# Kernel optimization log

Hardware: AMD Instinct MI355X
Metric: run time of the kernel (lower is better)

## Reference

```python
import jax, jax.numpy as jnp
import numpy as np
from jax import lax

D_MODEL = 512
D_STATE = 16
D_CONV = 4
EXPAND = 2
D_INNER = EXPAND * D_MODEL          # 1024
DT_RANK = (D_MODEL + 15) // 16      # 32 (ceil(d_model/16))
BATCH = 8
SEQLEN = 2048


def _mamba_params(key):
    ks = jax.random.split(key, 6)
    s = 0.02
    return {
        'in_w':   jax.random.normal(ks[0], (2 * D_INNER, D_MODEL)) * s,
        'conv_w': jax.random.normal(ks[1], (D_INNER, D_CONV)) * s,
        'conv_b': jnp.zeros((D_INNER,)),
        'xp_w':   jax.random.normal(ks[2], (DT_RANK + 2 * D_STATE, D_INNER)) * s,
        'dt_w':   jax.random.normal(ks[3], (D_INNER, DT_RANK)) * s,
        'dt_b':   jax.random.uniform(ks[4], (D_INNER,), minval=-4.0, maxval=-2.0),
        'A_log':  jnp.log(jnp.tile(jnp.arange(1, D_STATE + 1, dtype=jnp.float32), (D_INNER, 1))),
        'Dp':     jnp.ones((D_INNER,)),
        'out_w':  jax.random.normal(ks[5], (D_MODEL, D_INNER)) * s,
    }


def setup_inputs() -> dict:
    key = jax.random.key(0)
    kx, kf, kb, kl1, kl2 = jax.random.split(key, 5)
    pf = _mamba_params(kf)
    pb = _mamba_params(kb)
    inp = {'x': jax.random.normal(kx, (BATCH, SEQLEN, D_MODEL), dtype=jnp.float32)}
    for name, v in pf.items():
        inp['f_' + name] = v
    for name, v in pb.items():
        inp['b_' + name] = v
    inp['lin_w'] = jax.random.normal(kl1, (D_MODEL, 2 * D_MODEL)) * 0.02
    inp['lin_b'] = jnp.zeros((D_MODEL,))
    return inp


def _mamba(x, in_w, conv_w, conv_b, xp_w, dt_w, dt_b, A_log, Dp, out_w):
    # x: (B, L, D_MODEL)
    Bsz = x.shape[0]
    xz = x @ in_w.T                                  # (B, L, 2*D_INNER)
    xi, z = jnp.split(xz, 2, axis=-1)
    # causal depthwise conv over time
    xc = jnp.transpose(xi, (0, 2, 1))                # (B, D_INNER, L)
    xc = lax.conv_general_dilated(
        xc, conv_w[:, None, :], (1,), [(D_CONV - 1, 0)],
        feature_group_count=D_INNER)
    xi = jax.nn.silu(jnp.transpose(xc + conv_b[None, :, None], (0, 2, 1)))
    # input-dependent SSM params
    dbl = xi @ xp_w.T                                # (B, L, DT_RANK + 2*N)
    dt = jax.nn.softplus(dbl[..., :DT_RANK] @ dt_w.T + dt_b)    # (B, L, D_INNER)
    Bm = dbl[..., DT_RANK:DT_RANK + D_STATE]                    # (B, L, N)
    Cm = dbl[..., DT_RANK + D_STATE:]                           # (B, L, N)
    A = -jnp.exp(A_log)                                         # (D_INNER, N)

    def step(h, inp):
        dt_t, B_t, C_t, x_t = inp                    # (B,Di), (B,N), (B,N), (B,Di)
        h = jnp.exp(dt_t[..., None] * A) * h + (dt_t * x_t)[..., None] * B_t[:, None, :]
        y = jnp.einsum('bdn,bn->bd', h, C_t)
        return h, y

    xs = (jnp.swapaxes(dt, 0, 1), jnp.swapaxes(Bm, 0, 1),
          jnp.swapaxes(Cm, 0, 1), jnp.swapaxes(xi, 0, 1))
    h0 = jnp.zeros((Bsz, D_INNER, D_STATE), dtype=x.dtype)
    _, ys = lax.scan(step, h0, xs)                   # ys: (L, B, D_INNER)
    y = jnp.swapaxes(ys, 0, 1) + xi * Dp
    y = y * jax.nn.silu(z)
    return y @ out_w.T                               # (B, L, D_MODEL)


def reference(x,
              f_in_w, f_conv_w, f_conv_b, f_xp_w, f_dt_w, f_dt_b, f_A_log, f_Dp, f_out_w,
              b_in_w, b_conv_w, b_conv_b, b_xp_w, b_dt_w, b_dt_b, b_A_log, b_Dp, b_out_w,
              lin_w, lin_b):
    y_fwd = _mamba(x, f_in_w, f_conv_w, f_conv_b, f_xp_w, f_dt_w, f_dt_b, f_A_log, f_Dp, f_out_w)
    y_bwd = _mamba(x[:, ::-1, :], b_in_w, b_conv_w, b_conv_b, b_xp_w, b_dt_w, b_dt_b,
                   b_A_log, b_Dp, b_out_w)[:, ::-1, :]
    y = jnp.concatenate([y_fwd, y_bwd], axis=-1)     # (B, L, 2*D_MODEL)
    return y @ lin_w.T + lin_b
```

## Files before the change

### kernel.cpp

```cpp
#include <hip/hip_runtime.h>
#include <cmath>

#define LSEQ 2048
#define NBATCH 8

typedef __attribute__((ext_vector_type(8))) short short8;
typedef __attribute__((ext_vector_type(4))) float f32x4;

__device__ __forceinline__ float silu_f(float x) {
    return x * __builtin_amdgcn_rcpf(1.0f + __expf(-x));
}
__device__ __forceinline__ float softplus_f(float x) {
    return fmaxf(x, 0.0f) + __logf(1.0f + __expf(-fabsf(x)));
}
__device__ __forceinline__ unsigned short f2bf(float f) {
    unsigned int u = __float_as_uint(f);
    u += 0x7FFFu + ((u >> 16) & 1u);
    return (unsigned short)(u >> 16);
}
__device__ __forceinline__ float bf2f(unsigned short h) {
    return __uint_as_float(((unsigned int)h) << 16);
}
__device__ __forceinline__ void gload_lds16(const void* g, void* l) {
    __builtin_amdgcn_global_load_lds((const __attribute__((address_space(1))) void*)g,
                                     (__attribute__((address_space(3))) void*)l, 16, 0, 0);
}

#if defined(__has_builtin)
#if __has_builtin(__builtin_amdgcn_exp2f)
#define EXP2F(x) __builtin_amdgcn_exp2f(x)
#endif
#endif
#ifndef EXP2F
#define EXP2F(x) __expf((x) * 0.69314718055994531f)
#endif

struct GemmPair {
    const unsigned short* A[2];
    const unsigned short* A2[2];
    const unsigned short* W[2];
    const float* bias[2];
    void* C[2];
    unsigned short* aux[2];
};

template<int WGM, int WGN, int OMODE, int DK, int XTRA>
__global__ __launch_bounds__(WGM* WGN * 64) void gemm_mfma(GemmPair gp, int lda, int ldw,
                                                           int ldc, int K)
{
    constexpr int NW = WGM * WGN;
    constexpr int TM = WGM * 64, TN = WGN * 64;
    __shared__ unsigned short As[TM * 32];
    __shared__ unsigned short Bs[TN * 32];
    const int dir = blockIdx.z;
    const unsigned short* A  = gp.A[dir];
    const unsigned short* A2 = gp.A2[dir];
    const unsigned short* W  = gp.W[dir];
    const float* bias        = gp.bias[dir];
    void* Cout               = gp.C[dir];
    unsigned short* aux      = gp.aux[dir];

    const int tid = threadIdx.x;
    const int wave = tid >> 6, lane = tid & 63;
    const int wm = wave / WGN, wn = wave % WGN;
    const int m0 = blockIdx.x * TM, n0 = blockIdx.y * TN;
    const int l15 = lane & 15, l4 = lane >> 4;
    const int srow = lane >> 2, schunk = (lane & 3) * 8;

    f32x4 acc[4][4] = {};

    for (int k0 = 0; k0 < K; k0 += 32) {
        __syncthreads();
        for (int s = wave; s < TM / 16; s += NW) {
            const int gr = m0 + s * 16 + srow;
            const unsigned short* g;
            if (DK != 0 && k0 >= DK)
                g = A2 + (size_t)(gr ^ (LSEQ - 1)) * lda + (k0 - DK) + schunk;
            else
                g = A + (size_t)gr * lda + k0 + schunk;
            gload_lds16(g, (char*)As + (size_t)s * 1024);
        }
        for (int s = wave; s < TN / 16; s += NW) {
            const int gr = n0 + s * 16 + srow;
            const unsigned short* g = W + (size_t)gr * ldw + k0 + schunk;
            gload_lds16(g, (char*)Bs + (size_t)s * 1024);
        }
        __syncthreads();
        short8 af[4], bfr[4];
#pragma unroll
        for (int mi = 0; mi < 4; ++mi)
            af[mi] = *(const short8*)&As[(wm * 64 + mi * 16 + l15) * 32 + l4 * 8];
#pragma unroll
        for (int ni = 0; ni < 4; ++ni)
            bfr[ni] = *(const short8*)&Bs[(wn * 64 + ni * 16 + l15) * 32 + l4 * 8];
#pragma unroll
        for (int mi = 0; mi < 4; ++mi)
#pragma unroll
            for (int ni = 0; ni < 4; ++ni)
                acc[mi][ni] = __builtin_amdgcn_mfma_f32_16x16x32_bf16(af[mi], bfr[ni], acc[mi][ni], 0, 0, 0);
    }

#pragma unroll
    for (int mi = 0; mi < 4; ++mi)
#pragma unroll
        for (int ni = 0; ni < 4; ++ni)
#pragma unroll
            for (int r = 0; r < 4; ++r) {
                const int row = m0 + wm * 64 + mi * 16 + l4 * 4 + r;
                const int col = n0 + wn * 64 + ni * 16 + l15;
                float v = acc[mi][ni][r];
                if (bias) v += bias[col];
                if (OMODE & 1) ((unsigned short*)Cout)[(size_t)row * ldc + col] = f2bf(v);
                else           ((float*)Cout)[(size_t)row * ldc + col] = v;
                if (XTRA) { if (col < 32) aux[(size_t)row * 32 + col] = f2bf(v); }
            }
}

__global__ __launch_bounds__(256) void combine_k(
    const float* __restrict__ lin_w, const float* __restrict__ owf,
    const float* __restrict__ owb, unsigned short* __restrict__ Wcomb)
{
    const int dir = blockIdx.z;
    const float* ow = dir ? owb : owf;
    const int lane = threadIdx.x & 63;
    const int wave = threadIdx.x >> 6;
    const int n = blockIdx.y * 4 + wave;
    const int d = blockIdx.x * 256 + lane * 4;
    float4 acc = {0.f, 0.f, 0.f, 0.f};
    const float* lrow = lin_w + (size_t)n * 1024 + dir * 512;
    for (int j = 0; j < 512; ++j) {
        const float s = lrow[j];
        const float4 v = *(const float4*)&ow[(size_t)j * 1024 + d];
        acc.x = fmaf(s, v.x, acc.x); acc.y = fmaf(s, v.y, acc.y);
        acc.z = fmaf(s, v.z, acc.z); acc.w = fmaf(s, v.w, acc.w);
    }
    ushort4 o;
    o.x = f2bf(acc.x); o.y = f2bf(acc.y); o.z = f2bf(acc.z); o.w = f2bf(acc.w);
    *(ushort4*)&Wcomb[(size_t)n * 2048 + dir * 1024 + d] = o;
}

struct CvtArgs { const float* s[6]; unsigned short* d[6]; int n[6]; };
__global__ __launch_bounds__(256) void cvt_k(CvtArgs a)
{
    const int sid = blockIdx.y;
    const float* s = a.s[sid];
    unsigned short* d = a.d[sid];
    const int n4 = a.n[sid] >> 2;
    for (int i = blockIdx.x * 256 + threadIdx.x; i < n4; i += gridDim.x * 256) {
        const float4 v = ((const float4*)s)[i];
        ushort4 o; o.x = f2bf(v.x); o.y = f2bf(v.y); o.z = f2bf(v.z); o.w = f2bf(v.w);
        ((ushort4*)d)[i] = o;
    }
}
__global__ __launch_bounds__(256) void cvtx_k(const float* __restrict__ s,
                                              unsigned short* __restrict__ d, int n4)
{
    for (int i = blockIdx.x * 256 + threadIdx.x; i < n4; i += gridDim.x * 256) {
        const float4 v = ((const float4*)s)[i];
        ushort4 o; o.x = f2bf(v.x); o.y = f2bf(v.y); o.z = f2bf(v.z); o.w = f2bf(v.w);
        ((ushort4*)d)[i] = o;
    }
}

__global__ __launch_bounds__(256) void conv_silu_k(
    const unsigned short* __restrict__ xz_f, const float* __restrict__ cw_f,
    const float* __restrict__ cb_f, unsigned short* __restrict__ xi_f,
    const unsigned short* __restrict__ xz_b, const float* __restrict__ cw_b,
    const float* __restrict__ cb_b, unsigned short* __restrict__ xi_b)
{
    const int dir = blockIdx.y;
    const unsigned short* xz = dir ? xz_b : xz_f;
    const float* cw = dir ? cw_b : cw_f;
    const float* cb = dir ? cb_b : cb_f;
    unsigned short* xi = dir ? xi_b : xi_f;

    const int bt = blockIdx.x;
    const int b = bt >> 11;
    const int t = bt & (LSEQ - 1);
    const int d = threadIdx.x << 2;

    float w[4][4];
#pragma unroll
    for (int i = 0; i < 4; ++i) {
        const float4 wr = *(const float4*)&cw[(d + i) * 4];
        w[i][0] = wr.x; w[i][1] = wr.y; w[i][2] = wr.z; w[i][3] = wr.w;
    }
    float4 acc = *(const float4*)&cb[d];
#pragma unroll
    for (int k = 0; k < 4; ++k) {
        const int row = dir ? (LSEQ - 1 - t) + 3 - k : t - 3 + k;
        if ((unsigned)row < (unsigned)LSEQ) {
            const ushort4 v = *(const ushort4*)&xz[(size_t)(b * LSEQ + row) * 2048 + d];
            acc.x += w[0][k] * bf2f(v.x); acc.y += w[1][k] * bf2f(v.y);
            acc.z += w[2][k] * bf2f(v.z); acc.w += w[3][k] * bf2f(v.w);
        }
    }
    ushort4 st;
    st.x = f2bf(silu_f(acc.x)); st.y = f2bf(silu_f(acc.y));
    st.z = f2bf(silu_f(acc.z)); st.w = f2bf(silu_f(acc.w));
    *(ushort4*)&xi[(size_t)(b * LSEQ + t) * 1024 + d] = st;
}

__device__ __forceinline__ float row_sum8(float x) {
    x += __int_as_float(__builtin_amdgcn_update_dpp(0, __float_as_int(x), 0xB1, 0xF, 0xF, true));
    x += __int_as_float(__builtin_amdgcn_update_dpp(0, __float_as_int(x), 0x4E, 0xF, 0xF, true));
    x += __int_as_float(__builtin_amdgcn_update_dpp(0, __float_as_int(x), 0x141, 0xF, 0xF, true));
    return x;
}

struct ScanPair {
    const unsigned short* dblh[2];
    const unsigned short* dtw[2];
    const float* dtb[2];
    unsigned short* xiy[2];
    const float* dbl[2];
    const unsigned short* xz[2];
    const float* Al[2];
    const float* Dp[2];
};

__global__ __launch_bounds__(256, 2) void scan_k(ScanPair sp)
{
    __shared__ float sxi[2][64][36];
    __shared__ float sdt[32][68], sdtx[32][68];
    __shared__ float sB2[8][140], sC2[8][140];
    __shared__ float sy[32][68];

    const int dir = blockIdx.z;
    const unsigned short* dblh = sp.dblh[dir];
    const unsigned short* dtw  = sp.dtw[dir];
    const float* dtb           = sp.dtb[dir];
    unsigned short* xiy        = sp.xiy[dir];
    const float* dbl           = sp.dbl[dir];
    const unsigned short* zz   = sp.xz[dir];
    const float* Al            = sp.Al[dir];
    const float* Dpp           = sp.Dp[dir];

    const int b = blockIdx.y, d0 = blockIdx.x << 5;
    const int tid = threadIdx.x;
    const int wave = tid >> 6, lane = tid & 63;
    const int l15 = lane & 15, l4 = lane >> 4;
    const int di = tid >> 3, np = tid & 7;
    const int lr = tid >> 2, lc = tid & 3;
    const bool lead = (np == 0);

    const float A0L = -expf(Al[(d0 + di) * 16 + np]) * 1.4426950408889634f;
    const float A1L = -expf(Al[(d0 + di) * 16 + np + 8]) * 1.4426950408889634f;

    const short8 dtwf0 = *(const short8*)&dtw[(size_t)(d0 + l15) * 32 + l4 * 8];
    const short8 dtwf1 = *(const short8*)&dtw[(size_t)(d0 + 16 + l15) * 32 + l4 * 8];
    const float dtb0 = dtb[d0 + l15], dtb1 = dtb[d0 + 16 + l15];

    float dpv[8];
#pragma unroll
    for (int i = 0; i < 8; ++i) dpv[i] = Dpp[d0 + lc * 8 + i];

    ushort4 pxi0, pxi1;
    float4 pB, pC;
    short8 pA;
    auto issue_loads = [&](int c) {
        const size_t r = (size_t)b * LSEQ + c * 64 + lr;
        pxi0 = *(const ushort4*)&xiy[r * 1024 + d0 + lc * 8];
        pxi1 = *(const ushort4*)&xiy[r * 1024 + d0 + lc * 8 + 4];
        pB   = *(const float4*)&dbl[r * 64 + 32 + lc * 4];
        pC   = *(const float4*)&dbl[r * 64 + 48 + lc * 4];
        pA   = *(const short8*)&dblh[(size_t)(b * LSEQ + c * 64 + wave * 16 + l15) * 32 + l4 * 8];
    };
    issue_loads(0);

    float h0 = 0.0f, h1 = 0.0f;
    for (int c = 0; c < LSEQ / 64; ++c) {
        const int t0 = c * 64;
        const int buf = c & 1;
        {
            float4 xa, xb;
            xa.x = bf2f(pxi0.x); xa.y = bf2f(pxi0.y); xa.z = bf2f(pxi0.z); xa.w = bf2f(pxi0.w);
            xb.x = bf2f(pxi1.x); xb.y = bf2f(pxi1.y); xb.z = bf2f(pxi1.z); xb.w = bf2f(pxi1.w);
            *(float4*)&sxi[buf][lr][lc * 8]     = xa;
            *(float4*)&sxi[buf][lr][lc * 8 + 4] = xb;
        }
        {
            const float bv[4] = {pB.x, pB.y, pB.z, pB.w};
            const float cv[4] = {pC.x, pC.y, pC.z, pC.w};
#pragma unroll
            for (int i = 0; i < 4; ++i) {
                const int n = lc * 4 + i;
                sB2[n & 7][lr * 2 + (n >> 3)] = bv[i];
                sC2[n & 7][lr * 2 + (n >> 3)] = cv[i];
            }
        }
        __syncthreads();
        {
            f32x4 z4 = {0.f, 0.f, 0.f, 0.f};
            f32x4 dacc0 = __builtin_amdgcn_mfma_f32_16x16x32_bf16(pA, dtwf0, z4, 0, 0, 0);
            f32x4 dacc1 = __builtin_amdgcn_mfma_f32_16x16x32_bf16(pA, dtwf1, z4, 0, 0, 0);
            const int tq = wave * 16 + l4 * 4;
            float4 xi0, xi1;
            xi0.x = sxi[buf][tq + 0][l15];      xi0.y = sxi[buf][tq + 1][l15];
            xi0.z = sxi[buf][tq + 2][l15];      xi0.w = sxi[buf][tq + 3][l15];
            xi1.x = sxi[buf][tq + 0][16 + l15]; xi1.y = sxi[buf][tq + 1][16 + l15];
            xi1.z = sxi[buf][tq + 2][16 + l15]; xi1.w = sxi[buf][tq + 3][16 + l15];
            float4 dv0, dv1, dx0, dx1;
            dv0.x = softplus_f(dacc0[0] + dtb0); dv0.y = softplus_f(dacc0[1] + dtb0);
            dv0.z = softplus_f(dacc0[2] + dtb0); dv0.w = softplus_f(dacc0[3] + dtb0);
            dv1.x = softplus_f(dacc1[0] + dtb1); dv1.y = softplus_f(dacc1[1] + dtb1);
            dv1.z = softplus_f(dacc1[2] + dtb1); dv1.w = softplus_f(dacc1[3] + dtb1);
            dx0.x = dv0.x * xi0.x; dx0.y = dv0.y * xi0.y;
            dx0.z = dv0.z * xi0.z; dx0.w = dv0.w * xi0.w;
            dx1.x = dv1.x * xi1.x; dx1.y = dv1.y * xi1.y;
            dx1.z = dv1.z * xi1.z; dx1.w = dv1.w * xi1.w;
            *(float4*)&sdt[l15][tq]       = dv0;
            *(float4*)&sdt[16 + l15][tq]  = dv1;
            *(float4*)&sdtx[l15][tq]      = dx0;
            *(float4*)&sdtx[16 + l15][tq] = dx1;
        }
        if (c + 1 < LSEQ / 64) issue_loads(c + 1);
        ushort4 pz0, pz1;
        {
            const int tz = dir ? (LSEQ - 1 - (t0 + lr)) : (t0 + lr);
            pz0 = *(const ushort4*)&zz[((size_t)b * LSEQ + tz) * 2048 + 1024 + d0 + lc * 8];
            pz1 = *(const ushort4*)&zz[((size_t)b * LSEQ + tz) * 2048 + 1024 + d0 + lc * 8 + 4];
        }
        __syncthreads();
#pragma unroll 4
        for (int tt = 0; tt < 64; tt += 4) {
            const float4 d4 = *(const float4*)&sdt[di][tt];
            const float4 u4 = *(const float4*)&sdtx[di][tt];
            const float4 bA = *(const float4*)&sB2[np][tt * 2];
            const float4 bB = *(const float4*)&sB2[np][tt * 2 + 4];
            const float4 cA = *(const float4*)&sC2[np][tt * 2];
            const float4 cB = *(const float4*)&sC2[np][tt * 2 + 4];
            float4 ppv;
            h0 = fmaf(EXP2F(d4.x * A0L), h0, u4.x * bA.x);
            h1 = fmaf(EXP2F(d4.x * A1L), h1, u4.x * bA.y);
            ppv.x = row_sum8(fmaf(h1, cA.y, h0 * cA.x));
            h0 = fmaf(EXP2F(d4.y * A0L), h0, u4.y * bA.z);
            h1 = fmaf(EXP2F(d4.y * A1L), h1, u4.y * bA.w);
            ppv.y = row_sum8(fmaf(h1, cA.w, h0 * cA.z));
            h0 = fmaf(EXP2F(d4.z * A0L), h0, u4.z * bB.x);
            h1 = fmaf(EXP2F(d4.z * A1L), h1, u4.z * bB.y);
            ppv.z = row_sum8(fmaf(h1, cB.y, h0 * cB.x));
            h0 = fmaf(EXP2F(d4.w * A0L), h0, u4.w * bB.z);
            h1 = fmaf(EXP2F(d4.w * A1L), h1, u4.w * bB.w);
            ppv.w = row_sum8(fmaf(h1, cB.w, h0 * cB.z));
            if (lead) *(float4*)&sy[di][tt] = ppv;
        }
        __syncthreads();
        {
            const size_t r = (size_t)b * LSEQ + t0 + lr;
            const float4 xa = *(const float4*)&sxi[buf][lr][lc * 8];
            const float4 xb = *(const float4*)&sxi[buf][lr][lc * 8 + 4];
            float yv[8];
#pragma unroll
            for (int i = 0; i < 8; ++i) yv[i] = sy[lc * 8 + i][lr];
            ushort4 s0, s1;
            s0.x = f2bf(fmaf(xa.x, dpv[0], yv[0]) * silu_f(bf2f(pz0.x)));
            s0.y = f2bf(fmaf(xa.y, dpv[1], yv[1]) * silu_f(bf2f(pz0.y)));
            s0.z = f2bf(fmaf(xa.z, dpv[2], yv[2]) * silu_f(bf2f(pz0.z)));
            s0.w = f2bf(fmaf(xa.w, dpv[3], yv[3]) * silu_f(bf2f(pz0.w)));
            s1.x = f2bf(fmaf(xb.x, dpv[4], yv[4]) * silu_f(bf2f(pz1.x)));
            s1.y = f2bf(fmaf(xb.y, dpv[5], yv[5]) * silu_f(bf2f(pz1.y)));
            s1.z = f2bf(fmaf(xb.z, dpv[6], yv[6]) * silu_f(bf2f(pz1.z)));
            s1.w = f2bf(fmaf(xb.w, dpv[7], yv[7]) * silu_f(bf2f(pz1.w)));
            *(ushort4*)&xiy[r * 1024 + d0 + lc * 8] = s0;
            *(ushort4*)&xiy[r * 1024 + d0 + lc * 8 + 4] = s1;
        }
    }
}

extern "C" void kernel_launch(void* const* d_in, const int* in_sizes, int n_in,
                              void* d_out, int out_size, void* d_ws, size_t ws_size,
                              hipStream_t stream)
{
    const float* x      = (const float*)d_in[0];
    const float* f_in_w = (const float*)d_in[1];
    const float* f_cw   = (const float*)d_in[2];
    const float* f_cb   = (const float*)d_in[3];
    const float* f_xp   = (const float*)d_in[4];
    const float* f_dtw  = (const float*)d_in[5];
    const float* f_dtb  = (const float*)d_in[6];
    const float* f_Al   = (const float*)d_in[7];
    const float* f_Dp   = (const float*)d_in[8];
    const float* f_ow   = (const float*)d_in[9];
    const float* b_in_w = (const float*)d_in[10];
    const float* b_cw   = (const float*)d_in[11];
    const float* b_cb   = (const float*)d_in[12];
    const float* b_xp   = (const float*)d_in[13];
    const float* b_dtw  = (const float*)d_in[14];
    const float* b_dtb  = (const float*)d_in[15];
    const float* b_Al   = (const float*)d_in[16];
    const float* b_Dp   = (const float*)d_in[17];
    const float* b_ow   = (const float*)d_in[18];
    const float* lin_w  = (const float*)d_in[19];
    const float* lin_b  = (const float*)d_in[20];
    float* out = (float*)d_out;

    char* p = (char*)d_ws;
    auto take = [&](size_t bytes) -> char* {
        char* r = p; p += (bytes + 255) & ~(size_t)255; return r;
    };

    unsigned short* wif  = (unsigned short*)take((size_t)2048 * 512 * 2);
    unsigned short* wib  = (unsigned short*)take((size_t)2048 * 512 * 2);
    unsigned short* wxf  = (unsigned short*)take((size_t)64 * 1024 * 2);
    unsigned short* wxb  = (unsigned short*)take((size_t)64 * 1024 * 2);
    unsigned short* wdtf = (unsigned short*)take((size_t)1024 * 32 * 2);
    unsigned short* wdtb = (unsigned short*)take((size_t)1024 * 32 * 2);
    unsigned short* wcmb = (unsigned short*)take((size_t)512 * 2048 * 2);

    const size_t used = (size_t)(p - (char*)d_ws);
    const size_t perRow = 1024 + 2 * (4096 + 2048 + 256 + 64);
    int G = 1;
    for (int g = 8; g >= 1; g >>= 1) {
        const size_t need = used + (size_t)g * LSEQ * perRow + 16384;
        if (need <= ws_size || g == 1) { G = g; break; }
    }

    CvtArgs ca;
    ca.s[0] = f_in_w; ca.d[0] = wif;  ca.n[0] = 2048 * 512;
    ca.s[1] = b_in_w; ca.d[1] = wib;  ca.n[1] = 2048 * 512;
    ca.s[2] = f_xp;   ca.d[2] = wxf;  ca.n[2] = 64 * 1024;
    ca.s[3] = b_xp;   ca.d[3] = wxb;  ca.n[3] = 64 * 1024;
    ca.s[4] = f_dtw;  ca.d[4] = wdtf; ca.n[4] = 1024 * 32;
    ca.s[5] = b_dtw;  ca.d[5] = wdtb; ca.n[5] = 1024 * 32;
    cvt_k<<<dim3(128, 6), 256, 0, stream>>>(ca);

    combine_k<<<dim3(4, 128, 2), 256, 0, stream>>>(lin_w, f_ow, b_ow, wcmb);

    char* pg0 = p;
    for (int g0 = 0; g0 < NBATCH; g0 += G) {
        const int Mg = G * LSEQ;
        p = pg0;
        unsigned short* xbf   = (unsigned short*)take((size_t)Mg * 512 * 2);
        unsigned short* xz_f  = (unsigned short*)take((size_t)Mg * 2048 * 2);
        unsigned short* xz_b  = (unsigned short*)take((size_t)Mg * 2048 * 2);
        unsigned short* xiy_f = (unsigned short*)take((size_t)Mg * 1024 * 2);
        unsigned short* xiy_b = (unsigned short*)take((size_t)Mg * 1024 * 2);
        float* dbl_f          = (float*)take((size_t)Mg * 64 * 4);
        float* dbl_b          = (float*)take((size_t)Mg * 64 * 4);
        unsigned short* dblh_f= (unsigned short*)take((size_t)Mg * 32 * 2);
        unsigned short* dblh_b= (unsigned short*)take((size_t)Mg * 32 * 2);

        const float* xg = x + (size_t)g0 * LSEQ * 512;
        float* outg = out + (size_t)g0 * LSEQ * 512;

        cvtx_k<<<dim3(512), 256, 0, stream>>>(xg, xbf, Mg * 512 / 4);

        GemmPair g1 = {};
        g1.A[0] = xbf; g1.A[1] = xbf; g1.W[0] = wif; g1.W[1] = wib;
        g1.C[0] = xz_f; g1.C[1] = xz_b;
        gemm_mfma<2,2,1,0,0><<<dim3(Mg/128, 16, 2), 256, 0, stream>>>(g1, 512, 512, 2048, 512);

        conv_silu_k<<<dim3(Mg, 2), 256, 0, stream>>>(xz_f, f_cw, f_cb, xiy_f,
                                                     xz_b, b_cw, b_cb, xiy_b);

        GemmPair g2 = {};
        g2.A[0] = xiy_f; g2.A[1] = xiy_b; g2.W[0] = wxf; g2.W[1] = wxb;
        g2.C[0] = dbl_f; g2.C[1] = dbl_b; g2.aux[0] = dblh_f; g2.aux[1] = dblh_b;
        gemm_mfma<4,1,0,0,1><<<dim3(Mg/256, 1, 2), 256, 0, stream>>>(g2, 1024, 1024, 64, 1024);

        ScanPair spp = {};
        spp.dblh[0] = dblh_f; spp.dblh[1] = dblh_b;
        spp.dtw[0] = wdtf;    spp.dtw[1] = wdtb;
        spp.dtb[0] = f_dtb;   spp.dtb[1] = b_dtb;
        spp.xiy[0] = xiy_f;   spp.xiy[1] = xiy_b;
        spp.dbl[0] = dbl_f;   spp.dbl[1] = dbl_b;
        spp.xz[0] = xz_f;     spp.xz[1] = xz_b;
        spp.Al[0] = f_Al;     spp.Al[1] = b_Al;
        spp.Dp[0] = f_Dp;     spp.Dp[1] = b_Dp;
        scan_k<<<dim3(32, G, 2), 256, 0, stream>>>(spp);

        GemmPair g5 = {};
        g5.A[0] = xiy_f; g5.A2[0] = xiy_b; g5.W[0] = wcmb;
        g5.bias[0] = lin_b; g5.C[0] = outg;
        gemm_mfma<2,2,0,1024,0><<<dim3(Mg/128, 4, 1), 256, 0, stream>>>(g5, 1024, 2048, 512, 2048);
    }
}
```

Measured before the change: 736.9 us.

## Split selective scan into two sequence halves with a correction pass

The sequential scan now splits each sequence into two halves processed by separate blocks, doubling the grid's parallelism. The second half starts from a zero state and writes its partial output and cumulative dt to fp32 scratch. A new fix kernel adds the first half's final-state contribution via exp2(A*cumdt) and applies the gating. Occupancy hints rise to four blocks per CU and the xi staging buffer shrinks to single-buffered bf16. The cost is extra global traffic for the fp32 scratch buffers, one more kernel launch, and higher workspace use, which can lower the batch group size G.

```diff
diff --git a/kernel.cpp b/kernel.cpp
--- a/kernel.cpp
+++ b/kernel.cpp
@@ -162,6 +162,18 @@
     }
 }
 
+__global__ __launch_bounds__(256) void alprep_k(const float* __restrict__ af,
+                                                const float* __restrict__ ab,
+                                                float* __restrict__ of,
+                                                float* __restrict__ ob)
+{
+    const int i = blockIdx.x * 256 + threadIdx.x;
+    if (i < 16384) {
+        of[i] = -expf(af[i]) * 1.4426950408889634f;
+        ob[i] = -expf(ab[i]) * 1.4426950408889634f;
+    }
+}
+
 __global__ __launch_bounds__(256) void conv_silu_k(
     const unsigned short* __restrict__ xz_f, const float* __restrict__ cw_f,
     const float* __restrict__ cb_f, unsigned short* __restrict__ xi_f,
@@ -217,11 +229,14 @@
     const unsigned short* xz[2];
     const float* Al[2];
     const float* Dp[2];
+    float* cumg[2];
+    float* yd[2];
+    float* he[2];
 };
 
-__global__ __launch_bounds__(256, 2) void scan_k(ScanPair sp)
-{
-    __shared__ float sxi[2][64][36];
+__global__ __launch_bounds__(256, 4) void scan_k(ScanPair sp)
+{
+    __shared__ unsigned short sxi[64][40];
     __shared__ float sdt[32][68], sdtx[32][68];
     __shared__ float sB2[8][140], sC2[8][140];
     __shared__ float sy[32][68];
@@ -235,8 +250,14 @@
     const unsigned short* zz   = sp.xz[dir];
     const float* Al            = sp.Al[dir];
     const float* Dpp           = sp.Dp[dir];
-
-    const int b = blockIdx.y, d0 = blockIdx.x << 5;
+    float* cumg                = sp.cumg[dir];
+    float* ydp                 = sp.yd[dir];
+    float* hep                 = sp.he[dir];
+
+    const int by = blockIdx.y;
+    const int b = by >> 1, part = by & 1;
+    const int rbase = b * LSEQ + part * (LSEQ / 2);
+    const int d0 = blockIdx.x << 5;
     const int tid = threadIdx.x;
     const int wave = tid >> 6, lane = tid & 63;
     const int l15 = lane & 15, l4 = lane >> 4;
@@ -259,26 +280,21 @@
     float4 pB, pC;
     short8 pA;
     auto issue_loads = [&](int c) {
-        const size_t r = (size_t)b * LSEQ + c * 64 + lr;
+        const size_t r = (size_t)rbase + c * 64 + lr;
         pxi0 = *(const ushort4*)&xiy[r * 1024 + d0 + lc * 8];
         pxi1 = *(const ushort4*)&xiy[r * 1024 + d0 + lc * 8 + 4];
         pB   = *(const float4*)&dbl[r * 64 + 32 + lc * 4];
         pC   = *(const float4*)&dbl[r * 64 + 48 + lc * 4];
-        pA   = *(const short8*)&dblh[(size_t)(b * LSEQ + c * 64 + wave * 16 + l15) * 32 + l4 * 8];
+        pA   = *(const short8*)&dblh[(size_t)(rbase + c * 64 + wave * 16 + l15) * 32 + l4 * 8];
     };
     issue_loads(0);
 
-    float h0 = 0.0f, h1 = 0.0f;
-    for (int c = 0; c < LSEQ / 64; ++c) {
+    constexpr int NT = (LSEQ / 2) / 64;
+    float h0 = 0.0f, h1 = 0.0f, cum = 0.0f;
+    for (int c = 0; c < NT; ++c) {
         const int t0 = c * 64;
-        const int buf = c & 1;
-        {
-            float4 xa, xb;
-            xa.x = bf2f(pxi0.x); xa.y = bf2f(pxi0.y); xa.z = bf2f(pxi0.z); xa.w = bf2f(pxi0.w);
-            xb.x = bf2f(pxi1.x); xb.y = bf2f(pxi1.y); xb.z = bf2f(pxi1.z); xb.w = bf2f(pxi1.w);
-            *(float4*)&sxi[buf][lr][lc * 8]     = xa;
-            *(float4*)&sxi[buf][lr][lc * 8 + 4] = xb;
-        }
+        *(ushort4*)&sxi[lr][lc * 8]     = pxi0;
+        *(ushort4*)&sxi[lr][lc * 8 + 4] = pxi1;
         {
             const float bv[4] = {pB.x, pB.y, pB.z, pB.w};
             const float cv[4] = {pC.x, pC.y, pC.z, pC.w};
@@ -296,10 +312,10 @@
             f32x4 dacc1 = __builtin_amdgcn_mfma_f32_16x16x32_bf16(pA, dtwf1, z4, 0, 0, 0);
             const int tq = wave * 16 + l4 * 4;
             float4 xi0, xi1;
-            xi0.x = sxi[buf][tq + 0][l15];      xi0.y = sxi[buf][tq + 1][l15];
-            xi0.z = sxi[buf][tq + 2][l15];      xi0.w = sxi[buf][tq + 3][l15];
-            xi1.x = sxi[buf][tq + 0][16 + l15]; xi1.y = sxi[buf][tq + 1][16 + l15];
-            xi1.z = sxi[buf][tq + 2][16 + l15]; xi1.w = sxi[buf][tq + 3][16 + l15];
+            xi0.x = bf2f(sxi[tq + 0][l15]);      xi0.y = bf2f(sxi[tq + 1][l15]);
+            xi0.z = bf2f(sxi[tq + 2][l15]);      xi0.w = bf2f(sxi[tq + 3][l15]);
+            xi1.x = bf2f(sxi[tq + 0][16 + l15]); xi1.y = bf2f(sxi[tq + 1][16 + l15]);
+            xi1.z = bf2f(sxi[tq + 2][16 + l15]); xi1.w = bf2f(sxi[tq + 3][16 + l15]);
             float4 dv0, dv1, dx0, dx1;
             dv0.x = softplus_f(dacc0[0] + dtb0); dv0.y = softplus_f(dacc0[1] + dtb0);
             dv0.z = softplus_f(dacc0[2] + dtb0); dv0.w = softplus_f(dacc0[3] + dtb0);
@@ -314,13 +330,15 @@
             *(float4*)&sdtx[l15][tq]      = dx0;
             *(float4*)&sdtx[16 + l15][tq] = dx1;
         }
-        if (c + 1 < LSEQ / 64) issue_loads(c + 1);
-        ushort4 pz0, pz1;
-        {
-            const int tz = dir ? (LSEQ - 1 - (t0 + lr)) : (t0 + lr);
+        const ushort4 oxi0 = pxi0, oxi1 = pxi1;
+        ushort4 pz0 = {}, pz1 = {};
+        if (part == 0) {
+            const int tg = t0 + lr;
+            const int tz = dir ? (LSEQ - 1 - tg) : tg;
             pz0 = *(const ushort4*)&zz[((size_t)b * LSEQ + tz) * 2048 + 1024 + d0 + lc * 8];
             pz1 = *(const ushort4*)&zz[((size_t)b * LSEQ + tz) * 2048 + 1024 + d0 + lc * 8 + 4];
         }
+        if (c + 1 < NT) issue_loads(c + 1);
         __syncthreads();
 #pragma unroll 4
         for (int tt = 0; tt < 64; tt += 4) {
@@ -343,29 +361,98 @@
             h0 = fmaf(EXP2F(d4.w * A0L), h0, u4.w * bB.z);
             h1 = fmaf(EXP2F(d4.w * A1L), h1, u4.w * bB.w);
             ppv.w = row_sum8(fmaf(h1, cB.w, h0 * cB.z));
+            if (part) {
+                const float c0 = cum + d4.x, c1 = c0 + d4.y;
+                const float c2 = c1 + d4.z, c3 = c2 + d4.w;
+                cum = c3;
+                if (lead) {
+                    float* cg = &cumg[(size_t)(b * (LSEQ / 2) + t0 + tt) * 1024 + d0 + di];
+                    cg[0] = c0; cg[1024] = c1; cg[2048] = c2; cg[3072] = c3;
+                }
+            }
             if (lead) *(float4*)&sy[di][tt] = ppv;
         }
         __syncthreads();
-        {
-            const size_t r = (size_t)b * LSEQ + t0 + lr;
-            const float4 xa = *(const float4*)&sxi[buf][lr][lc * 8];
-            const float4 xb = *(const float4*)&sxi[buf][lr][lc * 8 + 4];
-            float yv[8];
-#pragma unroll
-            for (int i = 0; i < 8; ++i) yv[i] = sy[lc * 8 + i][lr];
+        if (part == 0) {
+            const size_t r = (size_t)rbase + t0 + lr;
             ushort4 s0, s1;
-            s0.x = f2bf(fmaf(xa.x, dpv[0], yv[0]) * silu_f(bf2f(pz0.x)));
-            s0.y = f2bf(fmaf(xa.y, dpv[1], yv[1]) * silu_f(bf2f(pz0.y)));
-            s0.z = f2bf(fmaf(xa.z, dpv[2], yv[2]) * silu_f(bf2f(pz0.z)));
-            s0.w = f2bf(fmaf(xa.w, dpv[3], yv[3]) * silu_f(bf2f(pz0.w)));
-            s1.x = f2bf(fmaf(xb.x, dpv[4], yv[4]) * silu_f(bf2f(pz1.x)));
-            s1.y = f2bf(fmaf(xb.y, dpv[5], yv[5]) * silu_f(bf2f(pz1.y)));
-            s1.z = f2bf(fmaf(xb.z, dpv[6], yv[6]) * silu_f(bf2f(pz1.z)));
-            s1.w = f2bf(fmaf(xb.w, dpv[7], yv[7]) * silu_f(bf2f(pz1.w)));
+            s0.x = f2bf(fmaf(bf2f(oxi0.x), dpv[0], sy[lc * 8 + 0][lr]) * silu_f(bf2f(pz0.x)));
+            s0.y = f2bf(fmaf(bf2f(oxi0.y), dpv[1], sy[lc * 8 + 1][lr]) * silu_f(bf2f(pz0.y)));
+            s0.z = f2bf(fmaf(bf2f(oxi0.z), dpv[2], sy[lc * 8 + 2][lr]) * silu_f(bf2f(pz0.z)));
+            s0.w = f2bf(fmaf(bf2f(oxi0.w), dpv[3], sy[lc * 8 + 3][lr]) * silu_f(bf2f(pz0.w)));
+            s1.x = f2bf(fmaf(bf2f(oxi1.x), dpv[4], sy[lc * 8 + 4][lr]) * silu_f(bf2f(pz1.x)));
+            s1.y = f2bf(fmaf(bf2f(oxi1.y), dpv[5], sy[lc * 8 + 5][lr]) * silu_f(bf2f(pz1.y)));
+            s1.z = f2bf(fmaf(bf2f(oxi1.z), dpv[6], sy[lc * 8 + 6][lr]) * silu_f(bf2f(pz1.z)));
+            s1.w = f2bf(fmaf(bf2f(oxi1.w), dpv[7], sy[lc * 8 + 7][lr]) * silu_f(bf2f(pz1.w)));
             *(ushort4*)&xiy[r * 1024 + d0 + lc * 8] = s0;
             *(ushort4*)&xiy[r * 1024 + d0 + lc * 8 + 4] = s1;
-        }
-    }
+        } else {
+            const size_t pr = (size_t)(b * (LSEQ / 2) + t0 + lr) * 1024 + d0 + lc * 8;
+            float4 w0, w1;
+            w0.x = fmaf(bf2f(oxi0.x), dpv[0], sy[lc * 8 + 0][lr]);
+            w0.y = fmaf(bf2f(oxi0.y), dpv[1], sy[lc * 8 + 1][lr]);
+            w0.z = fmaf(bf2f(oxi0.z), dpv[2], sy[lc * 8 + 2][lr]);
+            w0.w = fmaf(bf2f(oxi0.w), dpv[3], sy[lc * 8 + 3][lr]);
+            w1.x = fmaf(bf2f(oxi1.x), dpv[4], sy[lc * 8 + 4][lr]);
+            w1.y = fmaf(bf2f(oxi1.y), dpv[5], sy[lc * 8 + 5][lr]);
+            w1.z = fmaf(bf2f(oxi1.z), dpv[6], sy[lc * 8 + 6][lr]);
+            w1.w = fmaf(bf2f(oxi1.w), dpv[7], sy[lc * 8 + 7][lr]);
+            *(float4*)&ydp[pr]     = w0;
+            *(float4*)&ydp[pr + 4] = w1;
+        }
+    }
+    if (part == 0) {
+        float* hh = &hep[((size_t)b * 1024 + d0 + di) * 16 + np];
+        hh[0] = h0; hh[8] = h1;
+    }
+}
+
+struct FixArgs {
+    const float* yd[2]; const float* cumg[2]; const float* he[2];
+    const float* al2[2]; const float* dbl[2]; const unsigned short* xz[2];
+    unsigned short* xiy[2];
+};
+__global__ __launch_bounds__(256) void fix_k(FixArgs a)
+{
+    const int dir = blockIdx.z;
+    const float* yd            = a.yd[dir];
+    const float* cumg          = a.cumg[dir];
+    const float* he            = a.he[dir];
+    const float* al2           = a.al2[dir];
+    const float* dbl           = a.dbl[dir];
+    const unsigned short* xz   = a.xz[dir];
+    unsigned short* xiy        = a.xiy[dir];
+
+    __shared__ float sAL[64][17], sHE[64][17];
+    __shared__ float sC[4][16];
+
+    const int tid = threadIdx.x;
+    const int d0 = blockIdx.x << 6;
+    const int r0 = blockIdx.y << 2;
+    const int b = r0 >> 10;
+    for (int i = tid; i < 1024; i += 256) {
+        const int dd = i >> 4, nn = i & 15;
+        sAL[dd][nn] = al2[(size_t)(d0 + dd) * 16 + nn];
+        sHE[dd][nn] = he[((size_t)b * 1024 + d0 + dd) * 16 + nn];
+    }
+    if (tid < 64) {
+        const int rr = tid >> 4, n = tid & 15;
+        sC[rr][n] = dbl[((size_t)b * LSEQ + (LSEQ / 2) + ((r0 + rr) & 1023)) * 64 + 48 + n];
+    }
+    __syncthreads();
+    const int rr = tid >> 6, d = tid & 63;
+    const int lrow = r0 + rr;
+    const int t = (lrow & 1023) + (LSEQ / 2);
+    const size_t grow = (size_t)b * LSEQ + t;
+    const float cv = cumg[(size_t)lrow * 1024 + d0 + d];
+    float corr = 0.f;
+#pragma unroll
+    for (int n = 0; n < 16; ++n)
+        corr = fmaf(sC[rr][n] * sHE[d][n], EXP2F(sAL[d][n] * cv), corr);
+    const float yv = yd[(size_t)lrow * 1024 + d0 + d] + corr;
+    const int tz = dir ? (LSEQ - 1 - t) : t;
+    const float z = bf2f(xz[((size_t)b * LSEQ + tz) * 2048 + 1024 + d0 + d]);
+    xiy[grow * 1024 + d0 + d] = f2bf(yv * silu_f(z));
 }
 
 extern "C" void kernel_launch(void* const* d_in, const int* in_sizes, int n_in,
@@ -407,12 +494,14 @@
     unsigned short* wdtf = (unsigned short*)take((size_t)1024 * 32 * 2);
     unsigned short* wdtb = (unsigned short*)take((size_t)1024 * 32 * 2);
     unsigned short* wcmb = (unsigned short*)take((size_t)512 * 2048 * 2);
+    float* al2f = (float*)take((size_t)1024 * 16 * 4);
+    float* al2b = (float*)take((size_t)1024 * 16 * 4);
 
     const size_t used = (size_t)(p - (char*)d_ws);
-    const size_t perRow = 1024 + 2 * (4096 + 2048 + 256 + 64);
+    const size_t perRow = 1024 + 2 * (4096 + 2048 + 256 + 64 + 2048 + 2048);
     int G = 1;
     for (int g = 8; g >= 1; g >>= 1) {
-        const size_t need = used + (size_t)g * LSEQ * perRow + 16384;
+        const size_t need = used + (size_t)g * LSEQ * perRow + (size_t)g * 2 * 1024 * 16 * 4 + 16384;
         if (need <= ws_size || g == 1) { G = g; break; }
     }
 
@@ -424,6 +513,8 @@
     ca.s[4] = f_dtw;  ca.d[4] = wdtf; ca.n[4] = 1024 * 32;
     ca.s[5] = b_dtw;  ca.d[5] = wdtb; ca.n[5] = 1024 * 32;
     cvt_k<<<dim3(128, 6), 256, 0, stream>>>(ca);
+
+    alprep_k<<<dim3(64), 256, 0, stream>>>(f_Al, b_Al, al2f, al2b);
 
     combine_k<<<dim3(4, 128, 2), 256, 0, stream>>>(lin_w, f_ow, b_ow, wcmb);
 
@@ -440,6 +531,12 @@
         float* dbl_b          = (float*)take((size_t)Mg * 64 * 4);
         unsigned short* dblh_f= (unsigned short*)take((size_t)Mg * 32 * 2);
         unsigned short* dblh_b= (unsigned short*)take((size_t)Mg * 32 * 2);
+        float* cum_f          = (float*)take((size_t)G * 1024 * 1024 * 4);
+        float* cum_b          = (float*)take((size_t)G * 1024 * 1024 * 4);
+        float* yd_f           = (float*)take((size_t)G * 1024 * 1024 * 4);
+        float* yd_b           = (float*)take((size_t)G * 1024 * 1024 * 4);
+        float* he_f           = (float*)take((size_t)G * 1024 * 16 * 4);
+        float* he_b           = (float*)take((size_t)G * 1024 * 16 * 4);
 
         const float* xg = x + (size_t)g0 * LSEQ * 512;
         float* outg = out + (size_t)g0 * LSEQ * 512;
@@ -468,7 +565,20 @@
         spp.xz[0] = xz_f;     spp.xz[1] = xz_b;
         spp.Al[0] = f_Al;     spp.Al[1] = b_Al;
         spp.Dp[0] = f_Dp;     spp.Dp[1] = b_Dp;
-        scan_k<<<dim3(32, G, 2), 256, 0, stream>>>(spp);
+        spp.cumg[0] = cum_f;  spp.cumg[1] = cum_b;
+        spp.yd[0] = yd_f;     spp.yd[1] = yd_b;
+        spp.he[0] = he_f;     spp.he[1] = he_b;
+        scan_k<<<dim3(32, G * 2, 2), 256, 0, stream>>>(spp);
+
+        FixArgs fa = {};
+        fa.yd[0] = yd_f;   fa.yd[1] = yd_b;
+        fa.cumg[0] = cum_f; fa.cumg[1] = cum_b;
+        fa.he[0] = he_f;   fa.he[1] = he_b;
+        fa.al2[0] = al2f;  fa.al2[1] = al2b;
+        fa.dbl[0] = dbl_f; fa.dbl[1] = dbl_b;
+        fa.xz[0] = xz_f;   fa.xz[1] = xz_b;
+        fa.xiy[0] = xiy_f; fa.xiy[1] = xiy_b;
+        fix_k<<<dim3(16, G * 256, 2), 256, 0, stream>>>(fa);
 
         GemmPair g5 = {};
         g5.A[0] = xiy_f; g5.A2[0] = xiy_b; g5.W[0] = wcmb;
```

Result: slower. 941.8 us (+27.8%).
